# Optimization experiments

Hardware: AMD Instinct MI355X
Metric: run time of the kernel (lower is better)

## Reference

```python
import jax, jax.numpy as jnp
import numpy as np

# ---- module config (init kwargs) ----
EMB = 256
HIDDEN = 256
L, H, P = 4, 8, 4
CH = HIDDEN // H
PADDING_MODE = "zeros"   # 'zeros' or 'border'
ALIGN_CORNERS = False
# feature pyramid level shapes (height, width), static
SHAPES = np.array([[128, 128], [64, 64], [32, 32], [16, 16]], dtype=np.int32)
LEVEL_STARTS = np.concatenate([[0], np.cumsum(SHAPES.prod(-1))[:-1]]).astype(np.int32)

B, N = 8, 1024
I = int(SHAPES.prod(-1).sum())  # 21760


def setup_inputs() -> dict:
    key = jax.random.key(0)
    ks = jax.random.split(key, 8)
    scale = 0.02
    return {
        "img": jax.random.normal(ks[0], (B, I, EMB), jnp.float32),
        "img_shapes": jnp.asarray(SHAPES),
        "queries": jax.random.normal(ks[1], (B, N, EMB), jnp.float32),
        "reference_points": jax.random.uniform(ks[2], (B, N, 2), dtype=jnp.float32),
        "W_img": jax.random.normal(ks[3], (EMB, HIDDEN), jnp.float32) * scale,
        "b_img": jnp.zeros((HIDDEN,), jnp.float32),
        "W_q": jax.random.normal(ks[4], (EMB, H * L * P * 3), jnp.float32) * scale,
        "b_q": jnp.zeros((H * L * P * 3,), jnp.float32),
        "W_out": jax.random.normal(ks[5], (HIDDEN, EMB), jnp.float32) * scale,
        "b_out": jnp.zeros((EMB,), jnp.float32),
    }


def _msda(img, points, attn):
    """Multiscale deformable attention core.
    img:    [B, I, H, CH] flattened pyramid features
    points: [B, N, H, L, P, 2] (x, y) in [0, 1]
    attn:   [B, N, H, L, P]
    returns [B, N, H, CH]
    """
    b, _, h_, ch = img.shape
    n = points.shape[1]
    img_t = img.transpose(0, 2, 1, 3)  # [B, H, I, CH]
    levels = []
    for l in range(L):
        hh, ww = int(SHAPES[l, 0]), int(SHAPES[l, 1])
        start = int(LEVEL_STARTS[l])
        p = points[:, :, :, l]  # [B, N, H, P, 2]
        # grid_sample pixel mapping (after the module's 2*p-1 normalization)
        if ALIGN_CORNERS:
            x = p[..., 0] * (ww - 1)
            y = p[..., 1] * (hh - 1)
        else:
            x = p[..., 0] * ww - 0.5
            y = p[..., 1] * hh - 0.5
        x0 = jnp.floor(x); y0 = jnp.floor(y)
        wx = x - x0;       wy = y - y0
        x0i = x0.astype(jnp.int32); y0i = y0.astype(jnp.int32)
        acc = jnp.zeros((b, h_, n * P, ch), img.dtype)
        corners = [
            (x0i,     y0i,     (1 - wx) * (1 - wy)),
            (x0i + 1, y0i,     wx * (1 - wy)),
            (x0i,     y0i + 1, (1 - wx) * wy),
            (x0i + 1, y0i + 1, wx * wy),
        ]
        for xi, yi, cw in corners:
            if PADDING_MODE == "zeros":
                valid = (xi >= 0) & (xi < ww) & (yi >= 0) & (yi < hh)
                cw = cw * valid.astype(cw.dtype)
            xc = jnp.clip(xi, 0, ww - 1)
            yc = jnp.clip(yi, 0, hh - 1)
            idx = start + yc * ww + xc                              # [B, N, H, P]
            idx_t = idx.transpose(0, 2, 1, 3).reshape(b, h_, n * P)  # [B, H, N*P]
            g = jnp.take_along_axis(img_t, idx_t[..., None], axis=2)  # [B, H, N*P, CH]
            cw_t = cw.transpose(0, 2, 1, 3).reshape(b, h_, n * P, 1)
            acc = acc + cw_t * g
        levels.append(acc.reshape(b, h_, n, P, ch))
    samples = jnp.stack(levels, axis=3)            # [B, H, N, L, P, CH]
    attn_t = attn.transpose(0, 2, 1, 3, 4)          # [B, H, N, L, P]
    return jnp.einsum("bhnlpc,bhnlp->bnhc", samples, attn_t)


def reference(img, img_shapes, queries, reference_points, W_img, b_img, W_q, b_q, W_out, b_out):
    b, i_, _ = img.shape
    n = queries.shape[1]
    qp = (queries @ W_q + b_q).reshape(b, n, H, L, P, 3)
    offsets = qp[..., :2]                            # [B, N, H, L, P, 2]
    attn = jax.nn.softmax(qp[..., 2].reshape(b, n, H, L * P), axis=-1).reshape(b, n, H, L, P)
    img_p = (img @ W_img + b_img).reshape(b, i_, H, CH)
    shapes_f = img_shapes.astype(jnp.float32)        # [L, 2] (h, w)
    # faithful to source: offsets / img_shapes[:, None, :]
    sampling_points = reference_points[:, :, None, None, None, :] + offsets / shapes_f[:, None, :]
    out = _msda(img_p, sampling_points, attn)        # [B, N, H, CH]
    return out.reshape(b, n, HIDDEN) @ W_out + b_out
```

## Files before the change

### kernel.cpp

```cpp
#include <hip/hip_runtime.h>
#include <type_traits>
#include <utility>

#define B_    8
#define NQ_   1024
#define I_    21760
#define EMB_  256
#define HID_  256
#define H_    8
#define CH_   32

typedef float  f32x4  __attribute__((ext_vector_type(4)));
typedef __bf16 bf16x8 __attribute__((ext_vector_type(8)));
typedef short  s16x8  __attribute__((ext_vector_type(8)));

template <typename V, typename = void>
struct bf16_mfma_native : std::false_type {};
template <typename V>
struct bf16_mfma_native<V, std::void_t<decltype(__builtin_amdgcn_mfma_f32_16x16x32_bf16(
    std::declval<V>(), std::declval<V>(), std::declval<f32x4>(), 0, 0, 0))>>
    : std::true_type {};

template <typename V>
__device__ __forceinline__ f32x4 mfma_dispatch(V a, V b, f32x4 c) {
  if constexpr (bf16_mfma_native<V>::value) {
    return __builtin_amdgcn_mfma_f32_16x16x32_bf16(a, b, c, 0, 0, 0);
  } else {
    return __builtin_amdgcn_mfma_f32_16x16x32_bf16(
        __builtin_bit_cast(s16x8, a), __builtin_bit_cast(s16x8, b), c, 0, 0, 0);
  }
}

__device__ __forceinline__ f32x4 MFMA(s16x8 a, s16x8 b, f32x4 c) {
  return mfma_dispatch(__builtin_bit_cast(bf16x8, a), __builtin_bit_cast(bf16x8, b), c);
}

__device__ __forceinline__ unsigned short f2bf(float f) {
  unsigned u = __float_as_uint(f);
  u += 0x7fffu + ((u >> 16) & 1u);
  return (unsigned short)(u >> 16);
}

template <int NS, int OUTM>
__global__ __launch_bounds__(512) void gemm_k256(
    const float* __restrict__ A, const float* __restrict__ W,
    const float* __restrict__ bias, void* __restrict__ Out,
    const int N, const int Mtiles) {
  __shared__ __align__(16) short lds[32 * 264];
  const int tid  = threadIdx.x;
  const int lane = tid & 63;
  const int wave = tid >> 6;
  const int quad = lane >> 4;
  const int ln   = lane & 15;

  s16x8 bfrag[NS][8];
  float bv[NS];
#pragma unroll
  for (int st = 0; st < NS; ++st) {
    const int ng = st * 128 + wave * 16 + ln;
    bv[st] = bias[ng];
#pragma unroll
    for (int ks = 0; ks < 8; ++ks) {
      s16x8 f;
#pragma unroll
      for (int j = 0; j < 8; ++j)
        f[j] = (short)f2bf(W[(ks * 32 + quad * 8 + j) * N + ng]);
      bfrag[st][ks] = f;
    }
  }

  const int sr = tid >> 4;
  const int sc = (tid & 15) * 16;

  int t = blockIdx.x;
  float4 v0, v1, v2, v3;
  if (t < Mtiles) {
    const float4* src = (const float4*)(A + ((size_t)t * 32 + sr) * 256 + sc);
    v0 = src[0]; v1 = src[1]; v2 = src[2]; v3 = src[3];
  }

  for (; t < Mtiles; t += gridDim.x) {
    {
      s16x8 p0, p1;
      p0[0] = (short)f2bf(v0.x); p0[1] = (short)f2bf(v0.y);
      p0[2] = (short)f2bf(v0.z); p0[3] = (short)f2bf(v0.w);
      p0[4] = (short)f2bf(v1.x); p0[5] = (short)f2bf(v1.y);
      p0[6] = (short)f2bf(v1.z); p0[7] = (short)f2bf(v1.w);
      p1[0] = (short)f2bf(v2.x); p1[1] = (short)f2bf(v2.y);
      p1[2] = (short)f2bf(v2.z); p1[3] = (short)f2bf(v2.w);
      p1[4] = (short)f2bf(v3.x); p1[5] = (short)f2bf(v3.y);
      p1[6] = (short)f2bf(v3.z); p1[7] = (short)f2bf(v3.w);
      *(s16x8*)&lds[sr * 264 + sc]     = p0;
      *(s16x8*)&lds[sr * 264 + sc + 8] = p1;
    }
    __syncthreads();

    {
      const int tn = t + gridDim.x;
      if (tn < Mtiles) {
        const float4* src = (const float4*)(A + ((size_t)tn * 32 + sr) * 256 + sc);
        v0 = src[0]; v1 = src[1]; v2 = src[2]; v3 = src[3];
      }
    }

    f32x4 acc[NS][2];
#pragma unroll
    for (int st = 0; st < NS; ++st) {
      acc[st][0] = f32x4{bv[st], bv[st], bv[st], bv[st]};
      acc[st][1] = acc[st][0];
    }
#pragma unroll
    for (int ks = 0; ks < 8; ++ks) {
      s16x8 a0 = *(const s16x8*)&lds[ln * 264 + ks * 32 + quad * 8];
      s16x8 a1 = *(const s16x8*)&lds[(ln + 16) * 264 + ks * 32 + quad * 8];
#pragma unroll
      for (int st = 0; st < NS; ++st) {
        acc[st][0] = MFMA(a0, bfrag[st][ks], acc[st][0]);
        acc[st][1] = MFMA(a1, bfrag[st][ks], acc[st][1]);
      }
    }
    const size_t rowBase = (size_t)t * 32;
    if constexpr (OUTM == 1) {
      const int tb  = (int)(rowBase / I_);
      const int ir0 = (int)(rowBase - (size_t)tb * I_);
      unsigned short* O = (unsigned short*)Out;
#pragma unroll
      for (int st = 0; st < NS; ++st) {
        const int ng = st * 128 + wave * 16 + ln;
        const int hh = ng >> 5, cc = ng & 31;
        const size_t pl = (size_t)(tb * 8 + hh) * I_;
#pragma unroll
        for (int rt = 0; rt < 2; ++rt) {
#pragma unroll
          for (int r = 0; r < 4; ++r) {
            const size_t i = pl + (size_t)(ir0 + rt * 16 + quad * 4 + r);
            O[i * 32 + cc] = f2bf(acc[st][rt][r]);
          }
        }
      }
    } else {
      float* O = (float*)Out;
#pragma unroll
      for (int st = 0; st < NS; ++st) {
        const int ng = st * 128 + wave * 16 + ln;
#pragma unroll
        for (int rt = 0; rt < 2; ++rt) {
#pragma unroll
          for (int r = 0; r < 4; ++r) {
            const size_t m = rowBase + rt * 16 + quad * 4 + r;
            O[m * N + ng] = acc[st][rt][r];
          }
        }
      }
    }
    __syncthreads();
  }
}

__global__ __launch_bounds__(128) void msda_kernel(
    const unsigned int* __restrict__ imgp,
    const float* __restrict__ qp, const float* __restrict__ refp,
    float* __restrict__ out) {
  __shared__ __align__(16) float sw[128][4];
  __shared__ __align__(16) int   sib[128][2];
  const int blk = blockIdx.x;
  const int x   = blk & 7;
  const int j   = blk >> 3;
  const int c   = ((j >> 7) << 3) | x;
  const int b   = c >> 3, h = c & 7;
  const int qg  = j & 127;
  const int tid = threadIdx.x;
  const int pl  = (b * 8 + h) * I_;

  {
    const int q8 = tid >> 4, lp = tid & 15, l = lp >> 2;
    const int ww = 128 >> l;
    const int start = (65536 - (65536 >> (2 * l))) / 3;
    const float invsh = __uint_as_float((unsigned)(120 + l) << 23);

    const int n   = (qg << 3) | q8;
    const int bid = (b << 10) | n;
    const float* qb = qp + (size_t)bid * 384 + h * 48 + lp * 3;
    const float ox = qb[0], oy = qb[1], z = qb[2];
    float m = z;
    m = fmaxf(m, __shfl_xor(m, 1, 16));
    m = fmaxf(m, __shfl_xor(m, 2, 16));
    m = fmaxf(m, __shfl_xor(m, 4, 16));
    m = fmaxf(m, __shfl_xor(m, 8, 16));
    float e = __expf(z - m);
    float s = e;
    s += __shfl_xor(s, 1, 16);
    s += __shfl_xor(s, 2, 16);
    s += __shfl_xor(s, 4, 16);
    s += __shfl_xor(s, 8, 16);
    const float a = e / s;

    const float rx = refp[bid * 2], ry = refp[bid * 2 + 1];
    const float px = (rx + ox * invsh) * (float)ww - 0.5f;
    const float py = (ry + oy * invsh) * (float)ww - 0.5f;
    const float x0f = floorf(px), y0f = floorf(py);
    const float wx = px - x0f, wy = py - y0f;
    const int x0 = (int)x0f, y0 = (int)y0f;

    const int xb = min(max(x0, 0), ww - 2);
    float u0 = 0.f, u1 = 0.f;
    if (x0 >= 0 && x0 < ww)         { if (x0 == xb)     u0 += 1.f - wx; else u1 += 1.f - wx; }
    if (x0 + 1 >= 0 && x0 + 1 < ww) { if (x0 + 1 == xb) u0 += wx;       else u1 += wx; }
    const float wy0 = (y0 >= 0     && y0 < ww)     ? a * (1.f - wy) : 0.f;
    const float wy1 = (y0 + 1 >= 0 && y0 + 1 < ww) ? a * wy         : 0.f;
    const int yc0 = min(max(y0, 0), ww - 1);
    const int yc1 = min(max(y0 + 1, 0), ww - 1);

    const int pb = pl + start + xb;
    sw[tid][0] = wy0 * u0; sw[tid][1] = wy0 * u1;
    sw[tid][2] = wy1 * u0; sw[tid][3] = wy1 * u1;
    sib[tid][0] = (pb + yc0 * ww) * 16;
    sib[tid][1] = (pb + yc1 * ww) * 16;
  }
  __syncthreads();

  const int q8 = tid >> 4, c2 = tid & 15;
  const int p  = c2 >> 3;
  const int cp = ((c2 & 7) << 1) + (p << 4);
  float a0 = 0.f, a1 = 0.f, a2 = 0.f, a3 = 0.f;
#pragma unroll
  for (int lp = 0; lp < 16; ++lp) {
    const float4 w4 = *(const float4*)sw[q8 * 16 + lp];
    const int2   ib = *(const int2*)sib[q8 * 16 + lp];
    const float w0 = p ? w4.y : w4.x;
    const float w1 = p ? w4.w : w4.z;
    const uint2 ua = *(const uint2*)&imgp[ib.x + cp];
    const uint2 ub = *(const uint2*)&imgp[ib.y + cp];
    a0 += w0 * __uint_as_float(ua.x << 16);
    a1 += w0 * __uint_as_float(ua.x & 0xffff0000u);
    a2 += w0 * __uint_as_float(ua.y << 16);
    a3 += w0 * __uint_as_float(ua.y & 0xffff0000u);
    a0 += w1 * __uint_as_float(ub.x << 16);
    a1 += w1 * __uint_as_float(ub.x & 0xffff0000u);
    a2 += w1 * __uint_as_float(ub.y << 16);
    a3 += w1 * __uint_as_float(ub.y & 0xffff0000u);
  }
  a0 += __shfl_xor(a0, 8);
  a1 += __shfl_xor(a1, 8);
  a2 += __shfl_xor(a2, 8);
  a3 += __shfl_xor(a3, 8);
  float2 r;
  r.x = p ? a2 : a0;
  r.y = p ? a3 : a1;
  const int bid = (b << 10) | (qg << 3) | q8;
  *(float2*)&out[(size_t)bid * 256 + h * 32 + ((c2 & 7) << 2) + (p << 1)] = r;
}

#define OFF_IMGP 0ULL
#define OFF_QP   89128960ULL
#define OFF_MSDA 101711872ULL
#define WS_NEEDED 110100480ULL

extern "C" void kernel_launch(void* const* d_in, const int* in_sizes, int n_in,
                              void* d_out, int out_size, void* d_ws, size_t ws_size,
                              hipStream_t stream) {
  const float* img     = (const float*)d_in[0];
  const float* queries = (const float*)d_in[2];
  const float* refp    = (const float*)d_in[3];
  const float* W_img   = (const float*)d_in[4];
  const float* b_img   = (const float*)d_in[5];
  const float* W_q     = (const float*)d_in[6];
  const float* b_q     = (const float*)d_in[7];
  const float* W_out   = (const float*)d_in[8];
  const float* b_out   = (const float*)d_in[9];

  if (ws_size < WS_NEEDED) return;

  char* ws = (char*)d_ws;
  unsigned short* imgp = (unsigned short*)(ws + OFF_IMGP);
  float* qp   = (float*)(ws + OFF_QP);
  float* msda = (float*)(ws + OFF_MSDA);

  hipLaunchKernelGGL((gemm_k256<3, 0>), dim3(256), dim3(512), 0, stream,
                     queries, W_q, b_q, (void*)qp, 384, B_ * NQ_ / 32);
  hipLaunchKernelGGL((gemm_k256<2, 1>), dim3(512), dim3(512), 0, stream,
                     img, W_img, b_img, (void*)imgp, 256, I_ * B_ / 32);
  hipLaunchKernelGGL(msda_kernel, dim3(B_ * NQ_ * H_ / 8), dim3(128), 0, stream,
                     (const unsigned int*)imgp, qp, refp, msda);
  hipLaunchKernelGGL((gemm_k256<2, 0>), dim3(256), dim3(512), 0, stream,
                     msda, W_out, b_out, d_out, 256, B_ * NQ_ / 32);
}
```

Measured before the change: 338.2 us.

## Fuse projections into one launch and fuse MSDA with output GEMM

Merges the image and query projection GEMMs into a single kernel whose block ranges pick the phase, and also pre-converts W_out to transposed bf16 there. The deformable sampling and the output projection now share one kernel: each block handles 16 queries of one batch across all heads, stages the sampled features in LDS as bf16 and runs MFMA against the bf16 W_out. This removes two launches and the fp32 intermediate round trip through global memory. In exchange the MSDA stage now runs only 512 blocks with larger LDS use, which lowers parallelism and latency hiding for the gather-bound sampling loop, and it adds a bf16 rounding of the sampled features before the output GEMM.

After: 334.4 us. About the same (-1.1%).

```diff
diff --git a/kernel.cpp b/kernel.cpp
--- a/kernel.cpp
+++ b/kernel.cpp
@@ -42,11 +42,11 @@
 }
 
 template <int NS, int OUTM>
-__global__ __launch_bounds__(512) void gemm_k256(
+__device__ __forceinline__ void gemm_phase(
     const float* __restrict__ A, const float* __restrict__ W,
     const float* __restrict__ bias, void* __restrict__ Out,
-    const int N, const int Mtiles) {
-  __shared__ __align__(16) short lds[32 * 264];
+    const int N, const int Mtiles, short* __restrict__ lds,
+    const int bid0, const int nblk) {
   const int tid  = threadIdx.x;
   const int lane = tid & 63;
   const int wave = tid >> 6;
@@ -72,14 +72,14 @@
   const int sr = tid >> 4;
   const int sc = (tid & 15) * 16;
 
-  int t = blockIdx.x;
+  int t = bid0;
   float4 v0, v1, v2, v3;
   if (t < Mtiles) {
     const float4* src = (const float4*)(A + ((size_t)t * 32 + sr) * 256 + sc);
     v0 = src[0]; v1 = src[1]; v2 = src[2]; v3 = src[3];
   }
 
-  for (; t < Mtiles; t += gridDim.x) {
+  for (; t < Mtiles; t += nblk) {
     {
       s16x8 p0, p1;
       p0[0] = (short)f2bf(v0.x); p0[1] = (short)f2bf(v0.y);
@@ -96,7 +96,7 @@
     __syncthreads();
 
     {
-      const int tn = t + gridDim.x;
+      const int tn = t + nblk;
       if (tn < Mtiles) {
         const float4* src = (const float4*)(A + ((size_t)tn * 32 + sr) * 256 + sc);
         v0 = src[0]; v1 = src[1]; v2 = src[2]; v3 = src[3];
@@ -157,104 +157,165 @@
   }
 }
 
-__global__ __launch_bounds__(128) void msda_kernel(
+__global__ __launch_bounds__(512) void proj_kernel(
+    const float* __restrict__ img, const float* __restrict__ queries,
+    const float* __restrict__ W_img, const float* __restrict__ b_img,
+    const float* __restrict__ W_q, const float* __restrict__ b_q,
+    const float* __restrict__ W_out,
+    unsigned short* __restrict__ imgp, float* __restrict__ qp,
+    unsigned short* __restrict__ wob) {
+  __shared__ __align__(16) short lds[32 * 264];
+  if (blockIdx.x < 512) {
+    gemm_phase<2, 1>(img, W_img, b_img, (void*)imgp, 256, (B_ * I_) / 32,
+                     lds, blockIdx.x, 512);
+  } else {
+    gemm_phase<3, 0>(queries, W_q, b_q, (void*)qp, 384, (B_ * NQ_) / 32,
+                     lds, (int)blockIdx.x - 512, 64);
+    const int t2 = ((int)blockIdx.x - 512) * 512 + (int)threadIdx.x;
+    const int col = t2 >> 7;
+    const int k   = (t2 << 1) & 255;
+    const unsigned lo = f2bf(W_out[(size_t)k * 256 + col]);
+    const unsigned hi = f2bf(W_out[(size_t)(k + 1) * 256 + col]);
+    ((unsigned*)wob)[t2] = lo | (hi << 16);
+  }
+}
+
+__global__ __launch_bounds__(256) void msda_out_kernel(
     const unsigned int* __restrict__ imgp,
     const float* __restrict__ qp, const float* __restrict__ refp,
+    const unsigned short* __restrict__ wob, const float* __restrict__ b_out,
     float* __restrict__ out) {
-  __shared__ __align__(16) float sw[128][4];
-  __shared__ __align__(16) int   sib[128][2];
+  __shared__ __align__(16) float sw[1024][4];
+  __shared__ __align__(16) int   sib[1024][2];
+  __shared__ __align__(16) short lA[16 * 264];
   const int blk = blockIdx.x;
-  const int x   = blk & 7;
-  const int j   = blk >> 3;
-  const int c   = ((j >> 7) << 3) | x;
-  const int b   = c >> 3, h = c & 7;
-  const int qg  = j & 127;
+  const int b   = blk & 7;
+  const int n0  = (blk >> 3) << 4;
   const int tid = threadIdx.x;
-  const int pl  = (b * 8 + h) * I_;
-
-  {
-    const int q8 = tid >> 4, lp = tid & 15, l = lp >> 2;
-    const int ww = 128 >> l;
-    const int start = (65536 - (65536 >> (2 * l))) / 3;
-    const float invsh = __uint_as_float((unsigned)(120 + l) << 23);
-
-    const int n   = (qg << 3) | q8;
-    const int bid = (b << 10) | n;
-    const float* qb = qp + (size_t)bid * 384 + h * 48 + lp * 3;
-    const float ox = qb[0], oy = qb[1], z = qb[2];
-    float m = z;
-    m = fmaxf(m, __shfl_xor(m, 1, 16));
-    m = fmaxf(m, __shfl_xor(m, 2, 16));
-    m = fmaxf(m, __shfl_xor(m, 4, 16));
-    m = fmaxf(m, __shfl_xor(m, 8, 16));
-    float e = __expf(z - m);
-    float s = e;
-    s += __shfl_xor(s, 1, 16);
-    s += __shfl_xor(s, 2, 16);
-    s += __shfl_xor(s, 4, 16);
-    s += __shfl_xor(s, 8, 16);
-    const float a = e / s;
-
-    const float rx = refp[bid * 2], ry = refp[bid * 2 + 1];
-    const float px = (rx + ox * invsh) * (float)ww - 0.5f;
-    const float py = (ry + oy * invsh) * (float)ww - 0.5f;
-    const float x0f = floorf(px), y0f = floorf(py);
-    const float wx = px - x0f, wy = py - y0f;
-    const int x0 = (int)x0f, y0 = (int)y0f;
-
-    const int xb = min(max(x0, 0), ww - 2);
-    float u0 = 0.f, u1 = 0.f;
-    if (x0 >= 0 && x0 < ww)         { if (x0 == xb)     u0 += 1.f - wx; else u1 += 1.f - wx; }
-    if (x0 + 1 >= 0 && x0 + 1 < ww) { if (x0 + 1 == xb) u0 += wx;       else u1 += wx; }
-    const float wy0 = (y0 >= 0     && y0 < ww)     ? a * (1.f - wy) : 0.f;
-    const float wy1 = (y0 + 1 >= 0 && y0 + 1 < ww) ? a * wy         : 0.f;
-    const int yc0 = min(max(y0, 0), ww - 1);
-    const int yc1 = min(max(y0 + 1, 0), ww - 1);
-
-    const int pb = pl + start + xb;
-    sw[tid][0] = wy0 * u0; sw[tid][1] = wy0 * u1;
-    sw[tid][2] = wy1 * u0; sw[tid][3] = wy1 * u1;
-    sib[tid][0] = (pb + yc0 * ww) * 16;
-    sib[tid][1] = (pb + yc1 * ww) * 16;
-  }
-  __syncthreads();
-
-  const int q8 = tid >> 4, c2 = tid & 15;
-  const int p  = c2 >> 3;
-  const int cp = ((c2 & 7) << 1) + (p << 4);
-  float a0 = 0.f, a1 = 0.f, a2 = 0.f, a3 = 0.f;
-#pragma unroll
-  for (int lp = 0; lp < 16; ++lp) {
-    const float4 w4 = *(const float4*)sw[q8 * 16 + lp];
-    const int2   ib = *(const int2*)sib[q8 * 16 + lp];
-    const float w0 = p ? w4.y : w4.x;
-    const float w1 = p ? w4.w : w4.z;
-    const uint2 ua = *(const uint2*)&imgp[ib.x + cp];
-    const uint2 ub = *(const uint2*)&imgp[ib.y + cp];
-    a0 += w0 * __uint_as_float(ua.x << 16);
-    a1 += w0 * __uint_as_float(ua.x & 0xffff0000u);
-    a2 += w0 * __uint_as_float(ua.y << 16);
-    a3 += w0 * __uint_as_float(ua.y & 0xffff0000u);
-    a0 += w1 * __uint_as_float(ub.x << 16);
-    a1 += w1 * __uint_as_float(ub.x & 0xffff0000u);
-    a2 += w1 * __uint_as_float(ub.y << 16);
-    a3 += w1 * __uint_as_float(ub.y & 0xffff0000u);
-  }
-  a0 += __shfl_xor(a0, 8);
-  a1 += __shfl_xor(a1, 8);
-  a2 += __shfl_xor(a2, 8);
-  a3 += __shfl_xor(a3, 8);
-  float2 r;
-  r.x = p ? a2 : a0;
-  r.y = p ? a3 : a1;
-  const int bid = (b << 10) | (qg << 3) | q8;
-  *(float2*)&out[(size_t)bid * 256 + h * 32 + ((c2 & 7) << 2) + (p << 1)] = r;
+
+  for (int half = 0; half < 2; ++half) {
+#pragma unroll
+    for (int it = 0; it < 4; ++it) {
+      const int item = it * 256 + tid;
+      const int lp = item & 15, gh = item >> 4;
+      const int q8 = gh >> 3, h = gh & 7;
+      const int l = lp >> 2;
+      const int ww = 128 >> l;
+      const int start = (65536 - (65536 >> (2 * l))) / 3;
+      const float invsh = __uint_as_float((unsigned)(120 + l) << 23);
+
+      const int n   = n0 + (half << 3) + q8;
+      const int bid = (b << 10) | n;
+      const float* qb = qp + (size_t)bid * 384 + h * 48 + lp * 3;
+      const float ox = qb[0], oy = qb[1], z = qb[2];
+      float m = z;
+      m = fmaxf(m, __shfl_xor(m, 1, 16));
+      m = fmaxf(m, __shfl_xor(m, 2, 16));
+      m = fmaxf(m, __shfl_xor(m, 4, 16));
+      m = fmaxf(m, __shfl_xor(m, 8, 16));
+      float e = __expf(z - m);
+      float s = e;
+      s += __shfl_xor(s, 1, 16);
+      s += __shfl_xor(s, 2, 16);
+      s += __shfl_xor(s, 4, 16);
+      s += __shfl_xor(s, 8, 16);
+      const float a = e / s;
+
+      const float rx = refp[bid * 2], ry = refp[bid * 2 + 1];
+      const float px = (rx + ox * invsh) * (float)ww - 0.5f;
+      const float py = (ry + oy * invsh) * (float)ww - 0.5f;
+      const float x0f = floorf(px), y0f = floorf(py);
+      const float wx = px - x0f, wy = py - y0f;
+      const int x0 = (int)x0f, y0 = (int)y0f;
+
+      const int xb = min(max(x0, 0), ww - 2);
+      float u0 = 0.f, u1 = 0.f;
+      if (x0 >= 0 && x0 < ww)         { if (x0 == xb)     u0 += 1.f - wx; else u1 += 1.f - wx; }
+      if (x0 + 1 >= 0 && x0 + 1 < ww) { if (x0 + 1 == xb) u0 += wx;       else u1 += wx; }
+      const float wy0 = (y0 >= 0     && y0 < ww)     ? a * (1.f - wy) : 0.f;
+      const float wy1 = (y0 + 1 >= 0 && y0 + 1 < ww) ? a * wy         : 0.f;
+      const int yc0 = min(max(y0, 0), ww - 1);
+      const int yc1 = min(max(y0 + 1, 0), ww - 1);
+
+      const int pb = (b * 8 + h) * I_ + start + xb;
+      sw[item][0] = wy0 * u0; sw[item][1] = wy0 * u1;
+      sw[item][2] = wy1 * u0; sw[item][3] = wy1 * u1;
+      sib[item][0] = (pb + yc0 * ww) * 16;
+      sib[item][1] = (pb + yc1 * ww) * 16;
+    }
+    __syncthreads();
+
+#pragma unroll
+    for (int it = 0; it < 4; ++it) {
+      const int item = it * 256 + tid;
+      const int c2 = item & 15, gh = item >> 4;
+      const int q8 = gh >> 3, h = gh & 7;
+      const int p  = c2 >> 3;
+      const int cp = ((c2 & 7) << 1) + (p << 4);
+      float a0 = 0.f, a1 = 0.f, a2 = 0.f, a3 = 0.f;
+#pragma unroll
+      for (int lp = 0; lp < 16; ++lp) {
+        const float4 w4 = *(const float4*)sw[gh * 16 + lp];
+        const int2   ib = *(const int2*)sib[gh * 16 + lp];
+        const float w0 = p ? w4.y : w4.x;
+        const float w1 = p ? w4.w : w4.z;
+        const uint2 ua = *(const uint2*)&imgp[ib.x + cp];
+        const uint2 ub = *(const uint2*)&imgp[ib.y + cp];
+        a0 += w0 * __uint_as_float(ua.x << 16);
+        a1 += w0 * __uint_as_float(ua.x & 0xffff0000u);
+        a2 += w0 * __uint_as_float(ua.y << 16);
+        a3 += w0 * __uint_as_float(ua.y & 0xffff0000u);
+        a0 += w1 * __uint_as_float(ub.x << 16);
+        a1 += w1 * __uint_as_float(ub.x & 0xffff0000u);
+        a2 += w1 * __uint_as_float(ub.y << 16);
+        a3 += w1 * __uint_as_float(ub.y & 0xffff0000u);
+      }
+      a0 += __shfl_xor(a0, 8);
+      a1 += __shfl_xor(a1, 8);
+      a2 += __shfl_xor(a2, 8);
+      a3 += __shfl_xor(a3, 8);
+      const float rx = p ? a2 : a0;
+      const float ry = p ? a3 : a1;
+      const int row = (half << 3) + q8;
+      const unsigned pr = (unsigned)f2bf(rx) | ((unsigned)f2bf(ry) << 16);
+      *(unsigned*)&lA[row * 264 + h * 32 + ((c2 & 7) << 2) + (p << 1)] = pr;
+    }
+    __syncthreads();
+  }
+
+  const int lane = tid & 63, wv = tid >> 6;
+  const int quad = lane >> 4, ln = lane & 15;
+  f32x4 acc[4];
+#pragma unroll
+  for (int s = 0; s < 4; ++s) {
+    const float bb = b_out[wv * 64 + s * 16 + ln];
+    acc[s] = f32x4{bb, bb, bb, bb};
+  }
+#pragma unroll
+  for (int ks = 0; ks < 8; ++ks) {
+    const s16x8 a = *(const s16x8*)&lA[ln * 264 + ks * 32 + quad * 8];
+#pragma unroll
+    for (int s = 0; s < 4; ++s) {
+      const int ng = wv * 64 + s * 16 + ln;
+      const s16x8 wf = *(const s16x8*)&wob[(size_t)ng * 256 + ks * 32 + quad * 8];
+      acc[s] = MFMA(a, wf, acc[s]);
+    }
+  }
+#pragma unroll
+  for (int s = 0; s < 4; ++s) {
+    const int ng = wv * 64 + s * 16 + ln;
+#pragma unroll
+    for (int r = 0; r < 4; ++r) {
+      const int m = quad * 4 + r;
+      out[(size_t)(b * 1024 + n0 + m) * 256 + ng] = acc[s][r];
+    }
+  }
 }
 
 #define OFF_IMGP 0ULL
 #define OFF_QP   89128960ULL
-#define OFF_MSDA 101711872ULL
-#define WS_NEEDED 110100480ULL
+#define OFF_WOB  101711872ULL
+#define WS_NEEDED 101842944ULL
 
 extern "C" void kernel_launch(void* const* d_in, const int* in_sizes, int n_in,
                               void* d_out, int out_size, void* d_ws, size_t ws_size,
@@ -273,15 +334,13 @@
 
   char* ws = (char*)d_ws;
   unsigned short* imgp = (unsigned short*)(ws + OFF_IMGP);
-  float* qp   = (float*)(ws + OFF_QP);
-  float* msda = (float*)(ws + OFF_MSDA);
-
-  hipLaunchKernelGGL((gemm_k256<3, 0>), dim3(256), dim3(512), 0, stream,
-                     queries, W_q, b_q, (void*)qp, 384, B_ * NQ_ / 32);
-  hipLaunchKernelGGL((gemm_k256<2, 1>), dim3(512), dim3(512), 0, stream,
-                     img, W_img, b_img, (void*)imgp, 256, I_ * B_ / 32);
-  hipLaunchKernelGGL(msda_kernel, dim3(B_ * NQ_ * H_ / 8), dim3(128), 0, stream,
-                     (const unsigned int*)imgp, qp, refp, msda);
-  hipLaunchKernelGGL((gemm_k256<2, 0>), dim3(256), dim3(512), 0, stream,
-                     msda, W_out, b_out, d_out, 256, B_ * NQ_ / 32);
-}
+  float* qp            = (float*)(ws + OFF_QP);
+  unsigned short* wob  = (unsigned short*)(ws + OFF_WOB);
+
+  hipLaunchKernelGGL(proj_kernel, dim3(576), dim3(512), 0, stream,
+                     img, queries, W_img, b_img, W_q, b_q, W_out,
+                     imgp, qp, wob);
+  hipLaunchKernelGGL(msda_out_kernel, dim3(512), dim3(256), 0, stream,
+                     (const unsigned int*)imgp, qp, refp, wob, b_out,
+                     (float*)d_out);
+}
```
